# Performance work log

Hardware: AMD Instinct MI355X
Metric: run time of the kernel (lower is better)

The kernel has to match this reference:

```python
import jax, jax.numpy as jnp
import numpy as np

D = 4096
N_HEAD = 32
KV_HEAD = 8
GS = D * KV_HEAD // N_HEAD  # 1024, kv projection width
B, S = 1, 2048


def setup_inputs() -> dict:
    key = jax.random.key(0)
    ks = jax.random.split(key, 10)
    sc = 0.02
    return {
        "x": jax.random.normal(ks[0], (B, S, D), dtype=jnp.float32),
        "y": jax.random.normal(ks[1], (B, S, D), dtype=jnp.float32),
        "Wq": jax.random.normal(ks[2], (D, D), dtype=jnp.float32) * sc,
        "bq": jax.random.normal(ks[3], (D,), dtype=jnp.float32) * sc,
        "Wk": jax.random.normal(ks[4], (D, GS), dtype=jnp.float32) * sc,
        "bk": jax.random.normal(ks[5], (GS,), dtype=jnp.float32) * sc,
        "Wv": jax.random.normal(ks[6], (D, GS), dtype=jnp.float32) * sc,
        "bv": jax.random.normal(ks[7], (GS,), dtype=jnp.float32) * sc,
        "Wo": jax.random.normal(ks[8], (D, D), dtype=jnp.float32) * sc,
        "bo": jax.random.normal(ks[9], (D,), dtype=jnp.float32) * sc,
        "n_head": N_HEAD,
        "kv_head": KV_HEAD,
    }


def reference(x, y, Wq, bq, Wk, bk, Wv, bv, Wo, bo, n_head, kv_head):
    b, s, d = x.shape
    hd = d // n_head              # per-head dim
    gvs = hd // 2                 # complex pairs per head (group_vector_size)
    q = (x @ Wq + bq).reshape(b, s, n_head, hd)
    k = (y @ Wk + bk).reshape(b, s, kv_head, hd)
    v = (y @ Wv + bv).reshape(b, s, kv_head, hd)

    # RoPE: phi = 1/5000**(i/gvs); angle[p, i] = phi[i] * p  (matrix.T in torch)
    phi = 1.0 / (5000.0 ** (jnp.arange(gvs, dtype=jnp.float32) / gvs))
    ang = jnp.arange(s, dtype=jnp.float32)[:, None] * phi[None, :]  # [S, gvs]
    cos = jnp.cos(ang)[None, :, None, :]  # [1,S,1,gvs]
    sin = jnp.sin(ang)[None, :, None, :]

    def rope(t):
        # interleaved pairs (t[...,2i], t[...,2i+1]) form complex numbers
        tr, ti = t[..., 0::2], t[..., 1::2]
        ro = tr * cos - ti * sin
        io = tr * sin + ti * cos
        return jnp.stack([ro, io], axis=-1).reshape(t.shape)

    q = rope(q)
    k = rope(k)

    # GQA: head h uses kv head h // (n_head // kv_head) -> repeat kv heads
    module = n_head // kv_head
    k = jnp.repeat(k, module, axis=2)  # [B,S,H,hd]
    v = jnp.repeat(v, module, axis=2)

    scores = jnp.einsum("bqhd,bkhd->bhqk", q, k) / jnp.sqrt(jnp.float32(hd))
    causal = jnp.tril(jnp.ones((s, s), dtype=bool))
    scores = jnp.where(causal[None, None], scores, -jnp.inf)
    attn = jax.nn.softmax(scores, axis=-1)
    out = jnp.einsum("bhqk,bkhd->bqhd", attn, v).reshape(b, s, d)
    return out @ Wo + bo
```

## Files before the change

kernel.cpp:

```cpp
#include <hip/hip_runtime.h>
#include <hip/hip_bf16.h>

typedef unsigned int uint32;
typedef unsigned short ushort16;
typedef __attribute__((ext_vector_type(8))) __bf16 bf16x8;
typedef __attribute__((ext_vector_type(4))) float f32x4;

__device__ __forceinline__ ushort16 f2bf(float f) {
    uint32 u = __float_as_uint(f);
    u += 0x7fff + ((u >> 16) & 1);
    return (ushort16)(u >> 16);
}
__device__ __forceinline__ uint32 pack2rn(float a, float b) {
    uint32 ua = __float_as_uint(a) + 0x8000u;
    uint32 ub = __float_as_uint(b) + 0x8000u;
    return __builtin_amdgcn_perm(ub, ua, 0x07060302);
}
__device__ __forceinline__ float blo(uint32 u) { return __uint_as_float(u << 16); }
__device__ __forceinline__ float bhi(uint32 u) { return __uint_as_float(u & 0xffff0000u); }

__device__ __forceinline__ void storeC(float v, float* p) { *p = v; }
__device__ __forceinline__ void storeC(float v, ushort16* p) { *p = f2bf(v); }

__device__ __forceinline__ void gload_lds16(const void* g, void* l) {
    __builtin_amdgcn_global_load_lds(
        (const __attribute__((address_space(1))) unsigned int*)g,
        (__attribute__((address_space(3))) unsigned int*)l, 16, 0, 0);
}

__global__ __launch_bounds__(256) void conv2_bf16(
    const float* __restrict__ X, const float* __restrict__ Y,
    ushort16* __restrict__ Xb, ushort16* __restrict__ Yb, int n8)
{
    int idx = blockIdx.x * blockDim.x + threadIdx.x;
    const float* S = (idx < n8) ? X : Y;
    ushort16*    D = (idx < n8) ? Xb : Yb;
    int i = (idx < n8) ? idx : idx - n8;
    if (i >= n8) return;
    float4 a = ((const float4*)S)[2 * i];
    float4 b = ((const float4*)S)[2 * i + 1];
    uint4 u;
    u.x = pack2rn(a.x, a.y); u.y = pack2rn(a.z, a.w);
    u.z = pack2rn(b.x, b.y); u.w = pack2rn(b.z, b.w);
    ((uint4*)D)[i] = u;
}

__global__ __launch_bounds__(256) void transpose_w_bf16(
    const float* __restrict__ Wq, const float* __restrict__ Wk,
    const float* __restrict__ Wv, ushort16* __restrict__ Wqt,
    ushort16* __restrict__ Wkvt)
{
    __shared__ float tile[64][65];
    const int yb = blockIdx.y;
    const float* W; ushort16* Wt; int N, n0;
    if (yb < 64)      { W = Wq; Wt = Wqt;  N = 4096; n0 = yb * 64; }
    else if (yb < 80) { W = Wk; Wt = Wkvt; N = 1024; n0 = (yb - 64) * 64; }
    else              { W = Wv; Wt = Wkvt + (size_t)1024 * 4096; N = 1024; n0 = (yb - 80) * 64; }
    const int k0 = blockIdx.x * 64;
#pragma unroll
    for (int it = 0; it < 16; ++it) {
        int idx = threadIdx.x + it * 256;
        int r = idx >> 6, c = idx & 63;
        tile[r][c] = W[(size_t)(k0 + r) * N + n0 + c];
    }
    __syncthreads();
#pragma unroll
    for (int it = 0; it < 8; ++it) {
        int idx = threadIdx.x + it * 256;
        int nr = idx >> 5, kp = idx & 31;
        uint32 u = pack2rn(tile[2 * kp][nr], tile[2 * kp + 1][nr]);
        *(uint32*)&Wt[(size_t)(n0 + nr) * 4096 + k0 + 2 * kp] = u;
    }
}

__global__ __launch_bounds__(256) void gemm_qkv(
    const ushort16* __restrict__ xb, const ushort16* __restrict__ yb,
    const ushort16* __restrict__ Wqt, const ushort16* __restrict__ Wkvt,
    const float* __restrict__ bq, const float* __restrict__ bk,
    const float* __restrict__ bv, float* __restrict__ Q,
    ushort16* __restrict__ KVb)
{
    __shared__ __align__(16) ushort16 As[128 * 64];
    __shared__ __align__(16) ushort16 Bs[128 * 64];

    const bool isQ = (blockIdx.x < 32);
    const ushort16* A = isQ ? xb : yb;
    const ushort16* B = isQ ? Wqt : Wkvt;
    const int N   = isQ ? 4096 : 2048;
    const int gn0 = (isQ ? (int)blockIdx.x : (int)blockIdx.x - 32) * 128;
    const int gm0 = blockIdx.y * 128;
    const int K = 4096;

    const int tid  = threadIdx.x;
    const int lane = tid & 63, wave = tid >> 6;
    const int quad = lane >> 4, m16 = lane & 15;
    const int wm = (wave >> 1) * 64, wn = (wave & 1) * 64;

    f32x4 acc[4][4];
#pragma unroll
    for (int i = 0; i < 4; ++i)
#pragma unroll
        for (int j = 0; j < 4; ++j) acc[i][j] = (f32x4){0.f, 0.f, 0.f, 0.f};

    const int rl = lane >> 3, cl = lane & 7;
    const int clog = cl ^ (rl & 7);
    const ushort16* Ag = A + (size_t)(gm0 + wave * 32 + rl) * K + clog * 8;
    const ushort16* Bg = B + (size_t)(gn0 + wave * 32 + rl) * K + clog * 8;
    char* AsW = (char*)As + wave * 4096;
    char* BsW = (char*)Bs + wave * 4096;

    for (int k0 = 0; k0 < K; k0 += 64) {
        __syncthreads();
#pragma unroll
        for (int i = 0; i < 4; ++i) {
            gload_lds16(Ag + (size_t)(8 * i) * K, AsW + i * 1024);
            gload_lds16(Bg + (size_t)(8 * i) * K, BsW + i * 1024);
        }
        Ag += 64; Bg += 64;
        __syncthreads();

#pragma unroll
        for (int s = 0; s < 2; ++s) {
            bf16x8 aF[4], bF[4];
            const int cr = s * 4 + quad;
#pragma unroll
            for (int i = 0; i < 4; ++i) {
                int r = wm + i * 16 + m16;
                aF[i] = *(const bf16x8*)&As[r * 64 + ((cr ^ (r & 7)) * 8)];
                int n = wn + i * 16 + m16;
                bF[i] = *(const bf16x8*)&Bs[n * 64 + ((cr ^ (n & 7)) * 8)];
            }
            __builtin_amdgcn_s_setprio(1);
#pragma unroll
            for (int i = 0; i < 4; ++i)
#pragma unroll
                for (int j = 0; j < 4; ++j)
                    acc[i][j] = __builtin_amdgcn_mfma_f32_16x16x32_bf16(
                        aF[i], bF[j], acc[i][j], 0, 0, 0);
            __builtin_amdgcn_s_setprio(0);
        }
    }

#pragma unroll
    for (int j = 0; j < 4; ++j) {
        int col = gn0 + wn + j * 16 + m16;
        float bb = isQ ? bq[col] : ((col < 1024) ? bk[col] : bv[col - 1024]);
#pragma unroll
        for (int i = 0; i < 4; ++i) {
            int row0 = gm0 + wm + i * 16 + quad * 4;
#pragma unroll
            for (int r = 0; r < 4; ++r) {
                float v = acc[i][j][r] + bb;
                if (isQ) Q[(size_t)(row0 + r) * 4096 + col] = v;
                else     KVb[(size_t)(row0 + r) * 2048 + col] = f2bf(v);
            }
        }
    }
}

template <typename OutT>
__global__ __launch_bounds__(256) void gemm_mfma(
    const ushort16* __restrict__ A, const ushort16* __restrict__ B,
    const float* __restrict__ b1, OutT* __restrict__ C, int N, int K)
{
    __shared__ __align__(16) ushort16 As[128 * 64];
    __shared__ __align__(16) ushort16 Bs[128 * 64];

    const int tid  = threadIdx.x;
    const int lane = tid & 63, wave = tid >> 6;
    const int quad = lane >> 4, m16 = lane & 15;
    const int wm = (wave >> 1) * 64, wn = (wave & 1) * 64;
    const int gm0 = blockIdx.y * 128, gn0 = blockIdx.x * 128;

    f32x4 acc[4][4];
#pragma unroll
    for (int i = 0; i < 4; ++i)
#pragma unroll
        for (int j = 0; j < 4; ++j) acc[i][j] = (f32x4){0.f, 0.f, 0.f, 0.f};

    const int rl = lane >> 3, cl = lane & 7;
    const int clog = cl ^ (rl & 7);
    const ushort16* Ag = A + (size_t)(gm0 + wave * 32 + rl) * K + clog * 8;
    const ushort16* Bg = B + (size_t)(gn0 + wave * 32 + rl) * K + clog * 8;
    char* AsW = (char*)As + wave * 4096;
    char* BsW = (char*)Bs + wave * 4096;

    for (int k0 = 0; k0 < K; k0 += 64) {
        __syncthreads();
#pragma unroll
        for (int i = 0; i < 4; ++i) {
            gload_lds16(Ag + (size_t)(8 * i) * K, AsW + i * 1024);
            gload_lds16(Bg + (size_t)(8 * i) * K, BsW + i * 1024);
        }
        Ag += 64; Bg += 64;
        __syncthreads();

#pragma unroll
        for (int s = 0; s < 2; ++s) {
            bf16x8 aF[4], bF[4];
            const int cr = s * 4 + quad;
#pragma unroll
            for (int i = 0; i < 4; ++i) {
                int r = wm + i * 16 + m16;
                aF[i] = *(const bf16x8*)&As[r * 64 + ((cr ^ (r & 7)) * 8)];
                int n = wn + i * 16 + m16;
                bF[i] = *(const bf16x8*)&Bs[n * 64 + ((cr ^ (n & 7)) * 8)];
            }
            __builtin_amdgcn_s_setprio(1);
#pragma unroll
            for (int i = 0; i < 4; ++i)
#pragma unroll
                for (int j = 0; j < 4; ++j)
                    acc[i][j] = __builtin_amdgcn_mfma_f32_16x16x32_bf16(
                        aF[i], bF[j], acc[i][j], 0, 0, 0);
            __builtin_amdgcn_s_setprio(0);
        }
    }

#pragma unroll
    for (int j = 0; j < 4; ++j) {
        int col = gn0 + wn + j * 16 + m16;
        float bb = b1[col];
#pragma unroll
        for (int i = 0; i < 4; ++i) {
            int row0 = gm0 + wm + i * 16 + quad * 4;
#pragma unroll
            for (int r = 0; r < 4; ++r)
                storeC(acc[i][j][r] + bb, C + (size_t)(row0 + r) * N + col);
        }
    }
}

__global__ void rope_kernel(const float* __restrict__ T,
                            ushort16* __restrict__ Qb,
                            ushort16* __restrict__ KVb, int S)
{
    int idx = blockIdx.x * blockDim.x + threadIdx.x;
    const int nq = S * 32 * 64;
    if (idx < nq) {
        int i   = idx & 63;
        int rem = idx >> 6;
        int s   = rem >> 5;
        float inv = powf(5000.0f, -(float)i / 64.0f);
        float ang = (float)s * inv;
        float cs = cosf(ang), sn = sinf(ang);
        const float sc = 0.08838834764831845f * 1.4426950408889634f;
        size_t base = (size_t)rem * 128 + 2 * i;
        float tr = T[base], ti = T[base + 1];
        *(uint32*)&Qb[base] = pack2rn((tr * cs - ti * sn) * sc,
                                      (tr * sn + ti * cs) * sc);
    } else {
        idx -= nq;
        if (idx >= S * 8 * 64) return;
        int i   = idx & 63;
        int rem = idx >> 6;
        int s   = rem >> 3, h = rem & 7;
        float inv = powf(5000.0f, -(float)i / 64.0f);
        float ang = (float)s * inv;
        float cs = cosf(ang), sn = sinf(ang);
        uint32* p = (uint32*)&KVb[(size_t)s * 2048 + h * 128 + 2 * i];
        uint32 u = *p;
        float tr = blo(u), ti = bhi(u);
        *p = pack2rn(tr * cs - ti * sn, tr * sn + ti * cs);
    }
}

__global__ __launch_bounds__(256) void flash_attn_kernel(
    const ushort16* __restrict__ Qb, const ushort16* __restrict__ KVb,
    ushort16* __restrict__ O)
{
    __shared__ __align__(16) ushort16 Ks[64 * 128];
    __shared__ __align__(16) ushort16 Vt[128 * 64];
    __shared__ __align__(16) ushort16 Ps[64 * 64];

    const int tid  = threadIdx.x;
    const int lane = tid & 63, wave = tid >> 6;
    const int quad = lane >> 4, m16 = lane & 15;
    const int g = (int)blockIdx.y, h = g, kvh = h >> 2;
    const int qi = (g & 16) ? (31 - (int)blockIdx.x) : (int)blockIdx.x;
    const int q0 = qi * 64;

    const ushort16* Kbase = KVb + kvh * 128;
    const ushort16* Vbase = KVb + 1024 + kvh * 128;

    bf16x8 qa[4];
    {
        const ushort16* qp = Qb + (size_t)(q0 + wave * 16 + m16) * 4096
                           + h * 128 + quad * 8;
#pragma unroll
        for (int ks = 0; ks < 4; ++ks)
            qa[ks] = *(const bf16x8*)(qp + ks * 32);
    }

    f32x4 acc_o[8];
#pragma unroll
    for (int t = 0; t < 8; ++t) acc_o[t] = (f32x4){0.f, 0.f, 0.f, 0.f};
    float m_i[4], l_i[4];
#pragma unroll
    for (int r = 0; r < 4; ++r) { m_i[r] = -1e30f; l_i[r] = 0.f; }

    for (int k0 = 0; k0 <= q0; k0 += 64) {
        __syncthreads();

#pragma unroll
        for (int it = 0; it < 4; ++it) {
            int idx = tid + it * 256;
            int row = idx >> 4, c = idx & 15;
            *(uint4*)&Ks[row * 128 + ((c ^ (row & 7)) * 8)] =
                *(const uint4*)(Kbase + (size_t)(k0 + row) * 2048 + c * 8);
        }
#pragma unroll
        for (int it = 0; it < 2; ++it) {
            int idx = tid + it * 256;
            int rp  = idx & 31;
            int dcb = (idx >> 5) * 8;
            const ushort16* p0 = Vbase + (size_t)(k0 + 2 * rp) * 2048 + dcb;
            uint4 a = *(const uint4*)p0;
            uint4 b = *(const uint4*)(p0 + 2048);
            uint32 aw[4] = {a.x, a.y, a.z, a.w}, bw[4] = {b.x, b.y, b.z, b.w};
            int cc = rp >> 2, cbase = 2 * (rp & 3);
#pragma unroll
            for (int t = 0; t < 4; ++t) {
                int d0 = dcb + 2 * t, d1 = d0 + 1;
                *(uint32*)&Vt[d0 * 64 + ((cc ^ (d0 & 7)) * 8) + cbase] =
                    __builtin_amdgcn_perm(bw[t], aw[t], 0x05040100);
                *(uint32*)&Vt[d1 * 64 + ((cc ^ (d1 & 7)) * 8) + cbase] =
                    __builtin_amdgcn_perm(bw[t], aw[t], 0x07060302);
            }
        }
        __syncthreads();

        f32x4 sacc[4];
#pragma unroll
        for (int j = 0; j < 4; ++j) sacc[j] = (f32x4){0.f, 0.f, 0.f, 0.f};
        __builtin_amdgcn_s_setprio(1);
#pragma unroll
        for (int ks = 0; ks < 4; ++ks) {
#pragma unroll
            for (int j = 0; j < 4; ++j) {
                int n = j * 16 + m16;
                bf16x8 kb = *(const bf16x8*)&Ks[n * 128 + (((ks * 4 + quad) ^ (n & 7)) * 8)];
                sacc[j] = __builtin_amdgcn_mfma_f32_16x16x32_bf16(qa[ks], kb, sacc[j], 0, 0, 0);
            }
        }
        __builtin_amdgcn_s_setprio(0);

        if (k0 == q0) {
            int qr = wave * 16 + quad * 4;
#pragma unroll
            for (int j = 0; j < 4; ++j) {
                int kvl = j * 16 + m16;
#pragma unroll
                for (int r = 0; r < 4; ++r)
                    if (kvl > qr + r) sacc[j][r] = -1e30f;
            }
        }

#pragma unroll
        for (int r = 0; r < 4; ++r) {
            float rm = fmaxf(fmaxf(sacc[0][r], sacc[1][r]), fmaxf(sacc[2][r], sacc[3][r]));
            rm = fmaxf(rm, __shfl_xor(rm, 1));
            rm = fmaxf(rm, __shfl_xor(rm, 2));
            rm = fmaxf(rm, __shfl_xor(rm, 4));
            rm = fmaxf(rm, __shfl_xor(rm, 8));
            float mnew = fmaxf(m_i[r], rm);
            float al = exp2f(m_i[r] - mnew);
            float rs = 0.f;
#pragma unroll
            for (int j = 0; j < 4; ++j) {
                float pv = exp2f(sacc[j][r] - mnew);
                sacc[j][r] = pv;
                rs += pv;
            }
            rs += __shfl_xor(rs, 1);
            rs += __shfl_xor(rs, 2);
            rs += __shfl_xor(rs, 4);
            rs += __shfl_xor(rs, 8);
            l_i[r] = l_i[r] * al + rs;
            m_i[r] = mnew;
            int q = wave * 16 + quad * 4 + r;
#pragma unroll
            for (int j = 0; j < 4; ++j) {
                int kv = j * 16 + m16;
                Ps[q * 64 + (((kv >> 3) ^ (q & 7)) * 8) + (kv & 7)] = f2bf(sacc[j][r]);
            }
#pragma unroll
            for (int t = 0; t < 8; ++t) acc_o[t][r] *= al;
        }

        int qrow = wave * 16 + m16;
#pragma unroll
        for (int ks2 = 0; ks2 < 2; ++ks2) {
            bf16x8 pa = *(const bf16x8*)&Ps[qrow * 64 + (((ks2 * 4 + quad) ^ (qrow & 7)) * 8)];
            __builtin_amdgcn_s_setprio(1);
#pragma unroll
            for (int t = 0; t < 8; ++t) {
                int d = t * 16 + m16;
                bf16x8 vb = *(const bf16x8*)&Vt[d * 64 + (((ks2 * 4 + quad) ^ (d & 7)) * 8)];
                acc_o[t] = __builtin_amdgcn_mfma_f32_16x16x32_bf16(pa, vb, acc_o[t], 0, 0, 0);
            }
            __builtin_amdgcn_s_setprio(0);
        }
    }

    ushort16* op = O + (size_t)(q0 + wave * 16 + quad * 4) * 4096 + h * 128 + m16;
#pragma unroll
    for (int r = 0; r < 4; ++r) {
        float inv = 1.0f / l_i[r];
#pragma unroll
        for (int t = 0; t < 8; ++t)
            op[(size_t)r * 4096 + t * 16] = f2bf(acc_o[t][r] * inv);
    }
}

extern "C" void kernel_launch(void* const* d_in, const int* in_sizes, int n_in,
                              void* d_out, int out_size, void* d_ws, size_t ws_size,
                              hipStream_t stream)
{
    const float* x  = (const float*)d_in[0];
    const float* y  = (const float*)d_in[1];
    const float* Wq = (const float*)d_in[2];
    const float* bq = (const float*)d_in[3];
    const float* Wk = (const float*)d_in[4];
    const float* bk = (const float*)d_in[5];
    const float* Wv = (const float*)d_in[6];
    const float* bv = (const float*)d_in[7];
    const float* Wo = (const float*)d_in[8];
    const float* bo = (const float*)d_in[9];
    float* out = (float*)d_out;

    const int S = 2048, D = 4096;
    const size_t MB = 1024 * 1024;

    char* ws = (char*)d_ws;
    ushort16* xb   = (ushort16*)(ws);
    ushort16* yb   = (ushort16*)(ws + 16 * MB);
    ushort16* Wqt  = (ushort16*)(ws + 32 * MB);
    ushort16* Wkvt = (ushort16*)(ws + 64 * MB);
    ushort16* Wot  = (ushort16*)(ws + 80 * MB);
    ushort16* KVb  = (ushort16*)(ws + 112 * MB);
    ushort16* Qb   = xb;
    ushort16* Ao   = yb;
    float*    Q    = out;

    const int n8 = S * D / 8;
    conv2_bf16<<<2 * n8 / 256, 256, 0, stream>>>(x, y, xb, yb, n8);
    transpose_w_bf16<<<dim3(64, 96), 256, 0, stream>>>(Wq, Wk, Wv, Wqt, Wkvt);
    {
    }
    transpose_w_bf16<<<dim3(64, 64), 256, 0, stream>>>(Wo, Wk, Wv, Wot, Wkvt + (size_t)2048 * 4096);

    gemm_qkv<<<dim3(48, 16), 256, 0, stream>>>(
        xb, yb, Wqt, Wkvt, bq, bk, bv, Q, KVb);

    rope_kernel<<<(S * 40 * 64) / 256, 256, 0, stream>>>(Q, Qb, KVb, S);

    flash_attn_kernel<<<dim3(32, 32), 256, 0, stream>>>(Qb, KVb, Ao);

    gemm_mfma<float><<<dim3(32, 16), 256, 0, stream>>>(
        Ao, Wot, bo, out, D, D);
}
```

Measured before the change: 706.0 us.

## Pre-transpose V globally, double-buffer K via async LDS loads, pair causal query tiles

V is transposed once into a global buffer inside the rope kernel. Flash attention now stages K (double-buffered) and V tiles with global_load_lds so the next block's loads overlap the current compute. Each workgroup handles a short and a long causal query tile (16x32 grid) to balance work. The prep kernels (x/y conversion plus the Wq/Wk/Wv/Wo transposes) are merged into one launch to cut launch overhead. This adds a global V transpose pass and manual vmcnt waits, which must match the issued load counts.

```diff
diff --git a/kernel.cpp b/kernel.cpp
--- a/kernel.cpp
+++ b/kernel.cpp
@@ -28,35 +28,38 @@
         (__attribute__((address_space(3))) unsigned int*)l, 16, 0, 0);
 }
 
-__global__ __launch_bounds__(256) void conv2_bf16(
-    const float* __restrict__ X, const float* __restrict__ Y,
-    ushort16* __restrict__ Xb, ushort16* __restrict__ Yb, int n8)
-{
-    int idx = blockIdx.x * blockDim.x + threadIdx.x;
-    const float* S = (idx < n8) ? X : Y;
-    ushort16*    D = (idx < n8) ? Xb : Yb;
-    int i = (idx < n8) ? idx : idx - n8;
-    if (i >= n8) return;
-    float4 a = ((const float4*)S)[2 * i];
-    float4 b = ((const float4*)S)[2 * i + 1];
-    uint4 u;
-    u.x = pack2rn(a.x, a.y); u.y = pack2rn(a.z, a.w);
-    u.z = pack2rn(b.x, b.y); u.w = pack2rn(b.z, b.w);
-    ((uint4*)D)[i] = u;
-}
-
-__global__ __launch_bounds__(256) void transpose_w_bf16(
+__global__ __launch_bounds__(256) void prep_kernel(
+    const float* __restrict__ x, const float* __restrict__ y,
     const float* __restrict__ Wq, const float* __restrict__ Wk,
-    const float* __restrict__ Wv, ushort16* __restrict__ Wqt,
-    ushort16* __restrict__ Wkvt)
+    const float* __restrict__ Wv, const float* __restrict__ Wo,
+    ushort16* __restrict__ xb, ushort16* __restrict__ yb,
+    ushort16* __restrict__ Wqt, ushort16* __restrict__ Wkvt,
+    ushort16* __restrict__ Wot)
 {
     __shared__ float tile[64][65];
-    const int yb = blockIdx.y;
+    const int b = blockIdx.x;
+    if (b < 8192) {
+        const int n8 = 1048576;
+        int idx = b * 256 + threadIdx.x;
+        const float* S = (idx < n8) ? x : y;
+        ushort16*    D = (idx < n8) ? xb : yb;
+        int i = (idx < n8) ? idx : idx - n8;
+        float4 a = ((const float4*)S)[2 * i];
+        float4 c = ((const float4*)S)[2 * i + 1];
+        uint4 u;
+        u.x = pack2rn(a.x, a.y); u.y = pack2rn(a.z, a.w);
+        u.z = pack2rn(c.x, c.y); u.w = pack2rn(c.z, c.w);
+        ((uint4*)D)[i] = u;
+        return;
+    }
+    int t = b - 8192;
+    int kblk = t & 63, sel = t >> 6;
     const float* W; ushort16* Wt; int N, n0;
-    if (yb < 64)      { W = Wq; Wt = Wqt;  N = 4096; n0 = yb * 64; }
-    else if (yb < 80) { W = Wk; Wt = Wkvt; N = 1024; n0 = (yb - 64) * 64; }
-    else              { W = Wv; Wt = Wkvt + (size_t)1024 * 4096; N = 1024; n0 = (yb - 80) * 64; }
-    const int k0 = blockIdx.x * 64;
+    if (sel < 64)      { W = Wq; Wt = Wqt;  N = 4096; n0 = sel * 64; }
+    else if (sel < 80) { W = Wk; Wt = Wkvt; N = 1024; n0 = (sel - 64) * 64; }
+    else if (sel < 96) { W = Wv; Wt = Wkvt + (size_t)1024 * 4096; N = 1024; n0 = (sel - 80) * 64; }
+    else               { W = Wo; Wt = Wot;  N = 4096; n0 = (sel - 96) * 64; }
+    const int k0 = kblk * 64;
 #pragma unroll
     for (int it = 0; it < 16; ++it) {
         int idx = threadIdx.x + it * 256;
@@ -86,7 +89,6 @@
     const bool isQ = (blockIdx.x < 32);
     const ushort16* A = isQ ? xb : yb;
     const ushort16* B = isQ ? Wqt : Wkvt;
-    const int N   = isQ ? 4096 : 2048;
     const int gn0 = (isQ ? (int)blockIdx.x : (int)blockIdx.x - 32) * 128;
     const int gm0 = blockIdx.y * 128;
     const int K = 4096;
@@ -231,13 +233,14 @@
     }
 }
 
-__global__ void rope_kernel(const float* __restrict__ T,
-                            ushort16* __restrict__ Qb,
-                            ushort16* __restrict__ KVb, int S)
+__global__ __launch_bounds__(256) void rope_vt_kernel(
+    const float* __restrict__ T, ushort16* __restrict__ Qb,
+    ushort16* __restrict__ KVb, ushort16* __restrict__ Vt)
 {
-    int idx = blockIdx.x * blockDim.x + threadIdx.x;
-    const int nq = S * 32 * 64;
-    if (idx < nq) {
+    __shared__ ushort16 tile[64][66];
+    const int b = blockIdx.x;
+    if (b < 16384) {
+        int idx = b * 256 + threadIdx.x;
         int i   = idx & 63;
         int rem = idx >> 6;
         int s   = rem >> 5;
@@ -249,9 +252,10 @@
         float tr = T[base], ti = T[base + 1];
         *(uint32*)&Qb[base] = pack2rn((tr * cs - ti * sn) * sc,
                                       (tr * sn + ti * cs) * sc);
-    } else {
-        idx -= nq;
-        if (idx >= S * 8 * 64) return;
+        return;
+    }
+    if (b < 20480) {
+        int idx = (b - 16384) * 256 + threadIdx.x;
         int i   = idx & 63;
         int rem = idx >> 6;
         int s   = rem >> 3, h = rem & 7;
@@ -262,155 +266,195 @@
         uint32 u = *p;
         float tr = blo(u), ti = bhi(u);
         *p = pack2rn(tr * cs - ti * sn, tr * sn + ti * cs);
+        return;
+    }
+    int t = b - 20480;
+    int s0 = (t >> 4) * 64, d0 = (t & 15) * 64;
+#pragma unroll
+    for (int it = 0; it < 2; ++it) {
+        int i = threadIdx.x + it * 256;
+        int r = i >> 3, c = (i & 7) * 8;
+        *(uint4*)&tile[r][c] = *(const uint4*)&KVb[(size_t)(s0 + r) * 2048 + 1024 + d0 + c];
+    }
+    __syncthreads();
+#pragma unroll
+    for (int it = 0; it < 2; ++it) {
+        int i = threadIdx.x + it * 256;
+        int dr = i >> 3, sc = (i & 7) * 8;
+        uint32 w[4];
+#pragma unroll
+        for (int q = 0; q < 4; ++q)
+            w[q] = (uint32)tile[sc + 2 * q][dr] | ((uint32)tile[sc + 2 * q + 1][dr] << 16);
+        *(uint4*)&Vt[(size_t)(d0 + dr) * 2048 + s0 + sc] = *(uint4*)w;
     }
 }
 
 __global__ __launch_bounds__(256) void flash_attn_kernel(
     const ushort16* __restrict__ Qb, const ushort16* __restrict__ KVb,
-    ushort16* __restrict__ O)
+    const ushort16* __restrict__ Vtg, ushort16* __restrict__ O)
 {
-    __shared__ __align__(16) ushort16 Ks[64 * 128];
-    __shared__ __align__(16) ushort16 Vt[128 * 64];
+    __shared__ __align__(16) ushort16 Kb[2][64 * 128];
+    __shared__ __align__(16) ushort16 Vs[128 * 64];
     __shared__ __align__(16) ushort16 Ps[64 * 64];
 
     const int tid  = threadIdx.x;
     const int lane = tid & 63, wave = tid >> 6;
     const int quad = lane >> 4, m16 = lane & 15;
-    const int g = (int)blockIdx.y, h = g, kvh = h >> 2;
-    const int qi = (g & 16) ? (31 - (int)blockIdx.x) : (int)blockIdx.x;
-    const int q0 = qi * 64;
+    const int h = (int)blockIdx.y, kvh = h >> 2;
 
     const ushort16* Kbase = KVb + kvh * 128;
-    const ushort16* Vbase = KVb + 1024 + kvh * 128;
-
-    bf16x8 qa[4];
-    {
-        const ushort16* qp = Qb + (size_t)(q0 + wave * 16 + m16) * 4096
-                           + h * 128 + quad * 8;
-#pragma unroll
-        for (int ks = 0; ks < 4; ++ks)
-            qa[ks] = *(const bf16x8*)(qp + ks * 32);
-    }
-
-    f32x4 acc_o[8];
-#pragma unroll
-    for (int t = 0; t < 8; ++t) acc_o[t] = (f32x4){0.f, 0.f, 0.f, 0.f};
-    float m_i[4], l_i[4];
-#pragma unroll
-    for (int r = 0; r < 4; ++r) { m_i[r] = -1e30f; l_i[r] = 0.f; }
-
-    for (int k0 = 0; k0 <= q0; k0 += 64) {
-        __syncthreads();
-
-#pragma unroll
-        for (int it = 0; it < 4; ++it) {
-            int idx = tid + it * 256;
-            int row = idx >> 4, c = idx & 15;
-            *(uint4*)&Ks[row * 128 + ((c ^ (row & 7)) * 8)] =
-                *(const uint4*)(Kbase + (size_t)(k0 + row) * 2048 + c * 8);
-        }
-#pragma unroll
-        for (int it = 0; it < 2; ++it) {
-            int idx = tid + it * 256;
-            int rp  = idx & 31;
-            int dcb = (idx >> 5) * 8;
-            const ushort16* p0 = Vbase + (size_t)(k0 + 2 * rp) * 2048 + dcb;
-            uint4 a = *(const uint4*)p0;
-            uint4 b = *(const uint4*)(p0 + 2048);
-            uint32 aw[4] = {a.x, a.y, a.z, a.w}, bw[4] = {b.x, b.y, b.z, b.w};
-            int cc = rp >> 2, cbase = 2 * (rp & 3);
-#pragma unroll
-            for (int t = 0; t < 4; ++t) {
-                int d0 = dcb + 2 * t, d1 = d0 + 1;
-                *(uint32*)&Vt[d0 * 64 + ((cc ^ (d0 & 7)) * 8) + cbase] =
-                    __builtin_amdgcn_perm(bw[t], aw[t], 0x05040100);
-                *(uint32*)&Vt[d1 * 64 + ((cc ^ (d1 & 7)) * 8) + cbase] =
-                    __builtin_amdgcn_perm(bw[t], aw[t], 0x07060302);
-            }
-        }
-        __syncthreads();
-
-        f32x4 sacc[4];
-#pragma unroll
-        for (int j = 0; j < 4; ++j) sacc[j] = (f32x4){0.f, 0.f, 0.f, 0.f};
-        __builtin_amdgcn_s_setprio(1);
-#pragma unroll
-        for (int ks = 0; ks < 4; ++ks) {
-#pragma unroll
-            for (int j = 0; j < 4; ++j) {
-                int n = j * 16 + m16;
-                bf16x8 kb = *(const bf16x8*)&Ks[n * 128 + (((ks * 4 + quad) ^ (n & 7)) * 8)];
-                sacc[j] = __builtin_amdgcn_mfma_f32_16x16x32_bf16(qa[ks], kb, sacc[j], 0, 0, 0);
-            }
-        }
-        __builtin_amdgcn_s_setprio(0);
-
-        if (k0 == q0) {
-            int qr = wave * 16 + quad * 4;
-#pragma unroll
-            for (int j = 0; j < 4; ++j) {
-                int kvl = j * 16 + m16;
-#pragma unroll
-                for (int r = 0; r < 4; ++r)
-                    if (kvl > qr + r) sacc[j][r] = -1e30f;
-            }
-        }
-
+    const ushort16* Vbase = Vtg + (size_t)(kvh * 128) * 2048;
+
+    const int rK = lane >> 4;
+    const ushort16* pKe = Kbase + (size_t)(wave * 16 + rK) * 2048
+                        + (((lane & 15) ^ rK) * 8);
+    const ushort16* pKo = Kbase + (size_t)(wave * 16 + 4 + rK) * 2048
+                        + (((lane & 15) ^ (4 + rK)) * 8);
+    const int rV = lane >> 3;
+    const ushort16* pV  = Vbase + (size_t)(wave * 32 + rV) * 2048
+                        + (((lane & 7) ^ rV) * 8);
+    char* ldsK0 = (char*)&Kb[0][0] + wave * 4096;
+    char* ldsK1 = (char*)&Kb[1][0] + wave * 4096;
+    char* ldsV  = (char*)&Vs[0]    + wave * 4096;
+
+#define STAGE_K(dst, kk) do {                                   \
+        const ushort16* _s0 = pKe + (size_t)(kk) * 2048;        \
+        const ushort16* _s1 = pKo + (size_t)(kk) * 2048;        \
+        gload_lds16(_s0,            (dst));                     \
+        gload_lds16(_s1,            (dst) + 1024);              \
+        gload_lds16(_s0 + 8 * 2048, (dst) + 2048);              \
+        gload_lds16(_s1 + 8 * 2048, (dst) + 3072);              \
+    } while (0)
+#define STAGE_V(kk) do {                                        \
+        const ushort16* _sv = pV + (kk);                        \
+        gload_lds16(_sv,             ldsV);                     \
+        gload_lds16(_sv +  8 * 2048, ldsV + 1024);              \
+        gload_lds16(_sv + 16 * 2048, ldsV + 2048);              \
+        gload_lds16(_sv + 24 * 2048, ldsV + 3072);              \
+    } while (0)
+
+    for (int pass = 0; pass < 2; ++pass) {
+        const int qi = pass ? (int)blockIdx.x : 31 - (int)blockIdx.x;
+        const int q0 = qi * 64;
+
+        bf16x8 qa[4];
+        {
+            const ushort16* qp = Qb + (size_t)(q0 + wave * 16 + m16) * 4096
+                               + h * 128 + quad * 8;
+#pragma unroll
+            for (int ks = 0; ks < 4; ++ks)
+                qa[ks] = *(const bf16x8*)(qp + ks * 32);
+        }
+
+        f32x4 acc_o[8];
+#pragma unroll
+        for (int t = 0; t < 8; ++t) acc_o[t] = (f32x4){0.f, 0.f, 0.f, 0.f};
+        float m_i[4], l_i[4];
+#pragma unroll
+        for (int r = 0; r < 4; ++r) { m_i[r] = -1e30f; l_i[r] = 0.f; }
+
+        int cur = 0;
+        STAGE_K(ldsK0, 0);
+
+        for (int k0 = 0; k0 <= q0; k0 += 64) {
+            __syncthreads();
+
+            STAGE_V(k0);
+            const bool pre = (k0 + 64 <= q0);
+            if (pre) STAGE_K(cur ? ldsK0 : ldsK1, k0 + 64);
+
+            const ushort16* Kcur = &Kb[cur][0];
+
+            f32x4 sacc[4];
+#pragma unroll
+            for (int j = 0; j < 4; ++j) sacc[j] = (f32x4){0.f, 0.f, 0.f, 0.f};
+            __builtin_amdgcn_s_setprio(1);
+#pragma unroll
+            for (int ks = 0; ks < 4; ++ks) {
+#pragma unroll
+                for (int j = 0; j < 4; ++j) {
+                    int n = j * 16 + m16;
+                    bf16x8 kb = *(const bf16x8*)&Kcur[n * 128 + (((ks * 4 + quad) ^ (n & 7)) * 8)];
+                    sacc[j] = __builtin_amdgcn_mfma_f32_16x16x32_bf16(qa[ks], kb, sacc[j], 0, 0, 0);
+                }
+            }
+            __builtin_amdgcn_s_setprio(0);
+
+            if (k0 == q0) {
+                int qr = wave * 16 + quad * 4;
+#pragma unroll
+                for (int j = 0; j < 4; ++j) {
+                    int kvl = j * 16 + m16;
+#pragma unroll
+                    for (int r = 0; r < 4; ++r)
+                        if (kvl > qr + r) sacc[j][r] = -1e30f;
+                }
+            }
+
+#pragma unroll
+            for (int r = 0; r < 4; ++r) {
+                float rm = fmaxf(fmaxf(sacc[0][r], sacc[1][r]), fmaxf(sacc[2][r], sacc[3][r]));
+                rm = fmaxf(rm, __shfl_xor(rm, 1));
+                rm = fmaxf(rm, __shfl_xor(rm, 2));
+                rm = fmaxf(rm, __shfl_xor(rm, 4));
+                rm = fmaxf(rm, __shfl_xor(rm, 8));
+                float mnew = fmaxf(m_i[r], rm);
+                float al = exp2f(m_i[r] - mnew);
+                float rs = 0.f;
+#pragma unroll
+                for (int j = 0; j < 4; ++j) {
+                    float pv = exp2f(sacc[j][r] - mnew);
+                    sacc[j][r] = pv;
+                    rs += pv;
+                }
+                rs += __shfl_xor(rs, 1);
+                rs += __shfl_xor(rs, 2);
+                rs += __shfl_xor(rs, 4);
+                rs += __shfl_xor(rs, 8);
+                l_i[r] = l_i[r] * al + rs;
+                m_i[r] = mnew;
+                int q = wave * 16 + quad * 4 + r;
+#pragma unroll
+                for (int j = 0; j < 4; ++j) {
+                    int kv = j * 16 + m16;
+                    Ps[q * 64 + (((kv >> 3) ^ (q & 7)) * 8) + (kv & 7)] = f2bf(sacc[j][r]);
+                }
+#pragma unroll
+                for (int t = 0; t < 8; ++t) acc_o[t][r] *= al;
+            }
+
+            if (pre) { asm volatile("s_waitcnt vmcnt(4)" ::: "memory"); }
+            else     { asm volatile("s_waitcnt vmcnt(0)" ::: "memory"); }
+            __builtin_amdgcn_sched_barrier(0);
+            __builtin_amdgcn_s_barrier();
+
+            int qrow = wave * 16 + m16;
+#pragma unroll
+            for (int ks2 = 0; ks2 < 2; ++ks2) {
+                bf16x8 pa = *(const bf16x8*)&Ps[qrow * 64 + (((ks2 * 4 + quad) ^ (qrow & 7)) * 8)];
+                __builtin_amdgcn_s_setprio(1);
+#pragma unroll
+                for (int t = 0; t < 8; ++t) {
+                    int d = t * 16 + m16;
+                    bf16x8 vb = *(const bf16x8*)&Vs[d * 64 + (((ks2 * 4 + quad) ^ (d & 7)) * 8)];
+                    acc_o[t] = __builtin_amdgcn_mfma_f32_16x16x32_bf16(pa, vb, acc_o[t], 0, 0, 0);
+                }
+                __builtin_amdgcn_s_setprio(0);
+            }
+            cur ^= 1;
+        }
+
+        ushort16* op = O + (size_t)(q0 + wave * 16 + quad * 4) * 4096 + h * 128 + m16;
 #pragma unroll
         for (int r = 0; r < 4; ++r) {
-            float rm = fmaxf(fmaxf(sacc[0][r], sacc[1][r]), fmaxf(sacc[2][r], sacc[3][r]));
-            rm = fmaxf(rm, __shfl_xor(rm, 1));
-            rm = fmaxf(rm, __shfl_xor(rm, 2));
-            rm = fmaxf(rm, __shfl_xor(rm, 4));
-            rm = fmaxf(rm, __shfl_xor(rm, 8));
-            float mnew = fmaxf(m_i[r], rm);
-            float al = exp2f(m_i[r] - mnew);
-            float rs = 0.f;
-#pragma unroll
-            for (int j = 0; j < 4; ++j) {
-                float pv = exp2f(sacc[j][r] - mnew);
-                sacc[j][r] = pv;
-                rs += pv;
-            }
-            rs += __shfl_xor(rs, 1);
-            rs += __shfl_xor(rs, 2);
-            rs += __shfl_xor(rs, 4);
-            rs += __shfl_xor(rs, 8);
-            l_i[r] = l_i[r] * al + rs;
-            m_i[r] = mnew;
-            int q = wave * 16 + quad * 4 + r;
-#pragma unroll
-            for (int j = 0; j < 4; ++j) {
-                int kv = j * 16 + m16;
-                Ps[q * 64 + (((kv >> 3) ^ (q & 7)) * 8) + (kv & 7)] = f2bf(sacc[j][r]);
-            }
-#pragma unroll
-            for (int t = 0; t < 8; ++t) acc_o[t][r] *= al;
-        }
-
-        int qrow = wave * 16 + m16;
-#pragma unroll
-        for (int ks2 = 0; ks2 < 2; ++ks2) {
-            bf16x8 pa = *(const bf16x8*)&Ps[qrow * 64 + (((ks2 * 4 + quad) ^ (qrow & 7)) * 8)];
-            __builtin_amdgcn_s_setprio(1);
-#pragma unroll
-            for (int t = 0; t < 8; ++t) {
-                int d = t * 16 + m16;
-                bf16x8 vb = *(const bf16x8*)&Vt[d * 64 + (((ks2 * 4 + quad) ^ (d & 7)) * 8)];
-                acc_o[t] = __builtin_amdgcn_mfma_f32_16x16x32_bf16(pa, vb, acc_o[t], 0, 0, 0);
-            }
-            __builtin_amdgcn_s_setprio(0);
-        }
-    }
-
-    ushort16* op = O + (size_t)(q0 + wave * 16 + quad * 4) * 4096 + h * 128 + m16;
-#pragma unroll
-    for (int r = 0; r < 4; ++r) {
-        float inv = 1.0f / l_i[r];
-#pragma unroll
-        for (int t = 0; t < 8; ++t)
-            op[(size_t)r * 4096 + t * 16] = f2bf(acc_o[t][r] * inv);
-    }
+            float inv = 1.0f / l_i[r];
+#pragma unroll
+            for (int t = 0; t < 8; ++t)
+                op[(size_t)r * 4096 + t * 16] = f2bf(acc_o[t][r] * inv);
+        }
+    }
+#undef STAGE_K
+#undef STAGE_V
 }
 
 extern "C" void kernel_launch(void* const* d_in, const int* in_sizes, int n_in,
@@ -429,7 +473,6 @@
     const float* bo = (const float*)d_in[9];
     float* out = (float*)d_out;
 
-    const int S = 2048, D = 4096;
     const size_t MB = 1024 * 1024;
 
     char* ws = (char*)d_ws;
@@ -439,24 +482,21 @@
     ushort16* Wkvt = (ushort16*)(ws + 64 * MB);
     ushort16* Wot  = (ushort16*)(ws + 80 * MB);
     ushort16* KVb  = (ushort16*)(ws + 112 * MB);
+    ushort16* Vtg  = (ushort16*)(ws + 120 * MB);
     ushort16* Qb   = xb;
     ushort16* Ao   = yb;
     float*    Q    = out;
 
-    const int n8 = S * D / 8;
-    conv2_bf16<<<2 * n8 / 256, 256, 0, stream>>>(x, y, xb, yb, n8);
-    transpose_w_bf16<<<dim3(64, 96), 256, 0, stream>>>(Wq, Wk, Wv, Wqt, Wkvt);
-    {
-    }
-    transpose_w_bf16<<<dim3(64, 64), 256, 0, stream>>>(Wo, Wk, Wv, Wot, Wkvt + (size_t)2048 * 4096);
+    prep_kernel<<<18432, 256, 0, stream>>>(x, y, Wq, Wk, Wv, Wo,
+                                           xb, yb, Wqt, Wkvt, Wot);
 
     gemm_qkv<<<dim3(48, 16), 256, 0, stream>>>(
         xb, yb, Wqt, Wkvt, bq, bk, bv, Q, KVb);
 
-    rope_kernel<<<(S * 40 * 64) / 256, 256, 0, stream>>>(Q, Qb, KVb, S);
-
-    flash_attn_kernel<<<dim3(32, 32), 256, 0, stream>>>(Qb, KVb, Ao);
+    rope_vt_kernel<<<20992, 256, 0, stream>>>(Q, Qb, KVb, Vtg);
+
+    flash_attn_kernel<<<dim3(16, 32), 256, 0, stream>>>(Qb, KVb, Vtg, Ao);
 
     gemm_mfma<float><<<dim3(32, 16), 256, 0, stream>>>(
-        Ao, Wot, bo, out, D, D);
-}
+        Ao, Wot, bo, out, 4096, 4096);
+}
```

New measurement: 574.1 us. -18.7%, faster.
